# Optimization experiments

Hardware: AMD Instinct MI355X
Metric: run time of the kernel (lower is better)

The kernel has to match this reference:

```python
import jax, jax.numpy as jnp
import numpy as np

S, IN, OUT = 2048, 512, 512
H, KV = 16, 4            # query heads, kv heads (cross-broadcast + averaged)
DQ = DK = DV = 64        # per-head embedding dims


def setup_inputs() -> dict:
    key = jax.random.key(0)
    ks = jax.random.split(key, 5)
    lim_in = 1.0 / np.sqrt(IN)
    lim_o = 1.0 / np.sqrt(H * DV)
    x = jax.random.normal(ks[0], (S, IN), dtype=jnp.float32)
    Wq = jax.random.uniform(ks[1], (H * DQ, IN), jnp.float32, -lim_in, lim_in)
    Wk = jax.random.uniform(ks[2], (KV * DK, IN), jnp.float32, -lim_in, lim_in)
    Wv = jax.random.uniform(ks[3], (KV * DV, IN), jnp.float32, -lim_in, lim_in)
    Wo = jax.random.uniform(ks[4], (OUT, H * DV), jnp.float32, -lim_o, lim_o)
    return {"x": x, "Wq": Wq, "Wk": Wk, "Wv": Wv, "Wo": Wo}


def reference(x, Wq, Wk, Wv, Wo):
    seq = x.shape[0]
    # projections (eqx.nn.Linear: y = W @ x, no bias)
    q = (x @ Wq.T).reshape(seq, H, DQ)    # [S, H, DQ]
    k = (x @ Wk.T).reshape(seq, KV, DK)   # [S, KV, DK]
    v = (x @ Wv.T).reshape(seq, KV, DV)   # [S, KV, DV]
    # cross-broadcast every kv head against every query head -> [KV, H, S, S]
    scores = jnp.einsum('shd,tkd->khst', q, k) / jnp.sqrt(jnp.asarray(DK, x.dtype))
    # NOTE: original applies causal mask whenever `mask is not None`; the
    # boolean flag is always passed, so masking is effectively always on.
    causal = jnp.tril(jnp.ones((seq, seq), dtype=bool))
    scores = jnp.where(causal, scores, -jnp.inf)
    w = jax.nn.softmax(scores, axis=-1)   # [KV, H, S, S]
    # attn @ V, then sum over kv heads and average by KV
    o = jnp.einsum('khst,tkd->shd', w, v) / KV  # [S, H, DV]
    return o.reshape(seq, H * DV) @ Wo.T        # [S, OUT]
```

## Files before the change

kernel.cpp:

```cpp
#include <hip/hip_runtime.h>
#include <hip/hip_bf16.h>

#define SEQ   2048
#define INF_  512
#define HQ    16
#define KVH   4
#define DH    64
#define NQ    (HQ*DH)
#define NKV   (KVH*DH)
#define OUTD  512

typedef short v8s __attribute__((ext_vector_type(8)));
typedef float v4f __attribute__((ext_vector_type(4)));

static __device__ __forceinline__ float bf2f(unsigned short u) {
    union { unsigned int i; float f; } c;
    c.i = ((unsigned int)u) << 16;
    return c.f;
}
static __device__ __forceinline__ unsigned short f2bf(float f) {
    union { float f; unsigned int i; } c; c.f = f;
    unsigned int lsb = (c.i >> 16) & 1u;
    c.i += 0x7fffu + lsb;
    return (unsigned short)(c.i >> 16);
}
static __device__ __forceinline__ unsigned int f2bf2(float lo, float hi) {
    union { __hip_bfloat162 h; unsigned int u; } c;
    c.h = __float22bfloat162_rn(make_float2(lo, hi));
    return c.u;
}
static __device__ __forceinline__ v8s pack8(v4f a, v4f b) {
    union { v8s s; uint4 u; } c;
    c.u = make_uint4(f2bf2(a[0], a[1]), f2bf2(a[2], a[3]),
                     f2bf2(b[0], b[1]), f2bf2(b[2], b[3]));
    return c.s;
}

static __device__ __forceinline__ void gll16(const void* g, void* l) {
    __builtin_amdgcn_global_load_lds(
        (const __attribute__((address_space(1))) void*)g,
        (__attribute__((address_space(3))) void*)l, 16, 0, 0);
}

#define QSCALE 0.180336880f

__global__ __launch_bounds__(256) void cast_all(
    const float* __restrict__ x,  const float* __restrict__ Wq,
    const float* __restrict__ Wk, const float* __restrict__ Wv,
    const float* __restrict__ Wo,
    unsigned short* __restrict__ xb,  unsigned short* __restrict__ Wqb,
    unsigned short* __restrict__ Wkb, unsigned short* __restrict__ Wvb,
    unsigned short* __restrict__ Wob)
{
    size_t i = ((size_t)blockIdx.x * 256 + threadIdx.x) * 8;
    const float* s; unsigned short* d; size_t off;
    if (i < 1048576)      { s = x;  d = xb;  off = i; }
    else if (i < 1572864) { s = Wq; d = Wqb; off = i - 1048576; }
    else if (i < 1703936) { s = Wk; d = Wkb; off = i - 1572864; }
    else if (i < 1835008) { s = Wv; d = Wvb; off = i - 1703936; }
    else                  { s = Wo; d = Wob; off = i - 1835008; }
    float4 a = *(const float4*)(s + off);
    float4 b = *(const float4*)(s + off + 4);
    *(uint4*)(d + off) = make_uint4(f2bf2(a.x, a.y), f2bf2(a.z, a.w),
                                    f2bf2(b.x, b.y), f2bf2(b.z, b.w));
}

__global__ __launch_bounds__(256, 4) void gemm_qkv(
    const unsigned short* __restrict__ xb,
    const unsigned short* __restrict__ Wqb,
    const unsigned short* __restrict__ Wkb,
    const unsigned short* __restrict__ Wvb,
    unsigned short* __restrict__ Qg,
    unsigned short* __restrict__ Kg,
    unsigned short* __restrict__ Vg)
{
    __shared__ unsigned short Asb[64][72];
    __shared__ unsigned short Bsb[64][72];

    const int m0 = blockIdx.x * 64;
    const int n0 = blockIdx.y * 64;

    const unsigned short* Bp; int role;
    if (n0 < NQ)            { Bp = Wqb + (size_t)n0 * INF_;              role = 0; }
    else if (n0 < NQ + NKV) { Bp = Wkb + (size_t)(n0 - NQ) * INF_;       role = 1; }
    else                    { Bp = Wvb + (size_t)(n0 - NQ - NKV) * INF_; role = 2; }

    const int tid = threadIdx.x;
    const int w = tid >> 6, lane = tid & 63;
    const int n = lane & 15, quad = lane >> 4;
    const int r0w = (w & 1) * 32, c0w = (w >> 1) * 32;
    const int sr = tid >> 2, skc = (tid & 3) * 16;

    v4f acc[2][2];
#pragma unroll
    for (int rt = 0; rt < 2; rt++)
#pragma unroll
        for (int ct = 0; ct < 2; ct++) acc[rt][ct] = (v4f){0.f,0.f,0.f,0.f};

    const unsigned short* ap = xb + (size_t)(m0 + sr) * INF_ + skc;
    const unsigned short* bp = Bp + (size_t)sr * INF_ + skc;

    uint4 pa0 = *(const uint4*)(ap),     pa1 = *(const uint4*)(ap + 8);
    uint4 pb0 = *(const uint4*)(bp),     pb1 = *(const uint4*)(bp + 8);

    for (int kb = 0; kb < INF_; kb += 64) {
        __syncthreads();
        *(uint4*)&Asb[sr][skc]     = pa0;
        *(uint4*)&Asb[sr][skc + 8] = pa1;
        *(uint4*)&Bsb[sr][skc]     = pb0;
        *(uint4*)&Bsb[sr][skc + 8] = pb1;
        __syncthreads();
        if (kb + 64 < INF_) {
            pa0 = *(const uint4*)(ap + kb + 64);
            pa1 = *(const uint4*)(ap + kb + 64 + 8);
            pb0 = *(const uint4*)(bp + kb + 64);
            pb1 = *(const uint4*)(bp + kb + 64 + 8);
        }
#pragma unroll
        for (int kk = 0; kk < 2; kk++) {
            v8s a0 = *(const v8s*)&Asb[r0w + n][kk * 32 + quad * 8];
            v8s a1 = *(const v8s*)&Asb[r0w + 16 + n][kk * 32 + quad * 8];
            v8s b0 = *(const v8s*)&Bsb[c0w + n][kk * 32 + quad * 8];
            v8s b1 = *(const v8s*)&Bsb[c0w + 16 + n][kk * 32 + quad * 8];
            acc[0][0] = __builtin_amdgcn_mfma_f32_16x16x32_bf16(a0, b0, acc[0][0], 0, 0, 0);
            acc[0][1] = __builtin_amdgcn_mfma_f32_16x16x32_bf16(a0, b1, acc[0][1], 0, 0, 0);
            acc[1][0] = __builtin_amdgcn_mfma_f32_16x16x32_bf16(a1, b0, acc[1][0], 0, 0, 0);
            acc[1][1] = __builtin_amdgcn_mfma_f32_16x16x32_bf16(a1, b1, acc[1][1], 0, 0, 0);
        }
    }

    const int t = m0 >> 6;
    if (role == 0) {
        unsigned short* base = Qg + ((size_t)(t * 16 + (n0 >> 6))) * 4096;
#pragma unroll
        for (int rt = 0; rt < 2; rt++)
#pragma unroll
            for (int ct = 0; ct < 2; ct++)
#pragma unroll
                for (int reg = 0; reg < 4; reg++) {
                    const int r = r0w + rt * 16 + quad * 4 + reg;
                    const int d = c0w + ct * 16 + n;
                    base[r * 64 + (((d >> 3) ^ (r & 7)) * 8) + (d & 7)] =
                        f2bf(acc[rt][ct][reg] * QSCALE);
                }
    } else if (role == 1) {
        const int g = (n0 - NQ) >> 6;
        unsigned short* base = Kg + ((size_t)(g * 32 + t)) * 4096;
#pragma unroll
        for (int rt = 0; rt < 2; rt++)
#pragma unroll
            for (int ct = 0; ct < 2; ct++)
#pragma unroll
                for (int reg = 0; reg < 4; reg++) {
                    const int r = r0w + rt * 16 + quad * 4 + reg;
                    const int d = c0w + ct * 16 + n;
                    base[r * 64 + (((d >> 3) ^ (r & 7)) * 8) + (d & 7)] =
                        f2bf(acc[rt][ct][reg]);
                }
    } else {
        const int g = (n0 - NQ - NKV) >> 6;
        unsigned short* base = Vg + ((size_t)(g * 32 + t)) * 4096;
#pragma unroll
        for (int rt = 0; rt < 2; rt++)
#pragma unroll
            for (int ct = 0; ct < 2; ct++) {
                const int jb_ = r0w + rt * 16 + quad * 4;
                const int d = c0w + ct * 16 + n;
                const int p = (jb_ & 32) + (((jb_ >> 2) & 3) * 8) + (((jb_ >> 4) & 1) * 4);
                *(uint2*)&base[d * 64 + (((p >> 3) ^ (d & 7)) * 8) + (p & 7)] =
                    make_uint2(f2bf2(acc[rt][ct][0], acc[rt][ct][1]),
                               f2bf2(acc[rt][ct][2], acc[rt][ct][3]));
            }
    }
}

__global__ __launch_bounds__(256, 4) void attn_mfma(
    const unsigned short* __restrict__ Qg,
    const unsigned short* __restrict__ Kg,
    const unsigned short* __restrict__ Vg,
    unsigned short* __restrict__ Oh)
{
    __shared__ unsigned short Ksb[2][4096];
    __shared__ unsigned short Vsb[2][4096];

    const int bx = blockIdx.x;
    const int h  = bx & 15;
    const int jj = (bx >> 4) & 15;
    const int g  = bx >> 8;
    const int jj2 = (jj + 8 * (g >> 1)) & 15;
    const int qi2 = (g & 1) ? (15 - jj2) : jj2;
    const int q0 = qi2 * 128;
    const int tid = threadIdx.x;
    const int w = tid >> 6, lane = tid & 63;
    const int n = lane & 15, quad = lane >> 4;
    const int r0 = w * 32;
    const int m7 = n & 7;
    const int ntile = 2 * qi2 + 2;

    {
        const size_t off = ((size_t)(g * 32)) * 4096 + w * 1024 + lane * 8;
        gll16(Kg + off,       &Ksb[0][w * 1024]);
        gll16(Kg + off + 512, &Ksb[0][w * 1024 + 512]);
        gll16(Vg + off,       &Vsb[0][w * 1024]);
        gll16(Vg + off + 512, &Vsb[0][w * 1024 + 512]);
    }

    v8s qf[2][2];
    {
        const unsigned short* tb =
            Qg + ((size_t)((2 * qi2 + (r0 >> 6)) * 16 + h)) * 4096 + (r0 & 63) * 64;
#pragma unroll
        for (int qt = 0; qt < 2; qt++) {
            const unsigned short* rp = tb + (qt * 16 + n) * 64;
            qf[qt][0] = *(const v8s*)(rp + (quad ^ m7) * 8);
            qf[qt][1] = *(const v8s*)(rp + ((quad + 4) ^ m7) * 8);
        }
    }

    float lst[2] = {0.f, 0.f};
    v4f Oacc[2][4];
#pragma unroll
    for (int qt = 0; qt < 2; qt++)
#pragma unroll
        for (int dt = 0; dt < 4; dt++) Oacc[qt][dt] = (v4f){0.f,0.f,0.f,0.f};
    const v4f z = (v4f){0.f,0.f,0.f,0.f};

    for (int tt = 0; tt < ntile; tt++) {
        const int buf = tt & 1;
        __syncthreads();
        if (tt + 1 < ntile) {
            const size_t off = ((size_t)(g * 32 + tt + 1)) * 4096 + w * 1024 + lane * 8;
            const int nb = buf ^ 1;
            gll16(Kg + off,       &Ksb[nb][w * 1024]);
            gll16(Kg + off + 512, &Ksb[nb][w * 1024 + 512]);
            gll16(Vg + off,       &Vsb[nb][w * 1024]);
            gll16(Vg + off + 512, &Vsb[nb][w * 1024 + 512]);
        }
        const int t0 = tt * 64;
        const bool do0 = (t0 <= q0 + r0 + 15);
        const bool do1 = (t0 <= q0 + r0 + 31);
        if (!do1) continue;

        const unsigned short* Kb = Ksb[buf];
        const unsigned short* Vb = Vsb[buf];

        v4f sc[2][4];
#pragma unroll
        for (int jt = 0; jt < 4; jt++) {
            const int kr = (jt * 16 + n) * 64;
            v8s kf0 = *(const v8s*)&Kb[kr + (quad ^ m7) * 8];
            v8s kf1 = *(const v8s*)&Kb[kr + ((quad + 4) ^ m7) * 8];
            if (do0) {
                v4f tq = __builtin_amdgcn_mfma_f32_16x16x32_bf16(kf0, qf[0][0], z, 0, 0, 0);
                sc[0][jt] = __builtin_amdgcn_mfma_f32_16x16x32_bf16(kf1, qf[0][1], tq, 0, 0, 0);
            }
            v4f t1 = __builtin_amdgcn_mfma_f32_16x16x32_bf16(kf0, qf[1][0], z, 0, 0, 0);
            sc[1][jt] = __builtin_amdgcn_mfma_f32_16x16x32_bf16(kf1, qf[1][1], t1, 0, 0, 0);
        }

#pragma unroll
        for (int qt = 0; qt < 2; qt++) {
            if (qt == 0 && !do0) continue;
            const int qg = q0 + r0 + qt * 16 + n;
            if (t0 + 63 > q0 + r0 + qt * 16) {
#pragma unroll
                for (int jt = 0; jt < 4; jt++) {
                    const int jg = t0 + jt * 16 + quad * 4;
#pragma unroll
                    for (int reg = 0; reg < 4; reg++)
                        sc[qt][jt][reg] = (jg + reg <= qg) ? sc[qt][jt][reg] : -INFINITY;
                }
            }
#pragma unroll
            for (int jt = 0; jt < 4; jt++) {
#pragma unroll
                for (int reg = 0; reg < 4; reg++) {
                    float p = __builtin_amdgcn_exp2f(sc[qt][jt][reg]);
                    sc[qt][jt][reg] = p;
                    lst[qt] += p;
                }
            }
        }

        v8s pf[2][2];
        if (do0) {
            pf[0][0] = pack8(sc[0][0], sc[0][1]);
            pf[0][1] = pack8(sc[0][2], sc[0][3]);
        }
        pf[1][0] = pack8(sc[1][0], sc[1][1]);
        pf[1][1] = pack8(sc[1][2], sc[1][3]);

#pragma unroll
        for (int dt = 0; dt < 4; dt++) {
            const int vr = (dt * 16 + n) * 64;
            v8s vf0 = *(const v8s*)&Vb[vr + (quad ^ m7) * 8];
            v8s vf1 = *(const v8s*)&Vb[vr + ((quad + 4) ^ m7) * 8];
            if (do0) {
                Oacc[0][dt] = __builtin_amdgcn_mfma_f32_16x16x32_bf16(vf0, pf[0][0], Oacc[0][dt], 0, 0, 0);
                Oacc[0][dt] = __builtin_amdgcn_mfma_f32_16x16x32_bf16(vf1, pf[0][1], Oacc[0][dt], 0, 0, 0);
            }
            Oacc[1][dt] = __builtin_amdgcn_mfma_f32_16x16x32_bf16(vf0, pf[1][0], Oacc[1][dt], 0, 0, 0);
            Oacc[1][dt] = __builtin_amdgcn_mfma_f32_16x16x32_bf16(vf1, pf[1][1], Oacc[1][dt], 0, 0, 0);
        }
    }

    unsigned short* Ohp = Oh + (size_t)g * ((size_t)SEQ * NQ);
#pragma unroll
    for (int qt = 0; qt < 2; qt++) {
        float L = lst[qt];
        L += __shfl_xor(L, 16);
        L += __shfl_xor(L, 32);
        const float inv = 0.25f / L;
        const int row = q0 + r0 + qt * 16 + n;
        unsigned short* dst = Ohp + (size_t)row * NQ + h * DH + quad * 4;
#pragma unroll
        for (int dt = 0; dt < 4; dt++) {
            uint2 pk = make_uint2(f2bf2(Oacc[qt][dt][0] * inv, Oacc[qt][dt][1] * inv),
                                  f2bf2(Oacc[qt][dt][2] * inv, Oacc[qt][dt][3] * inv));
            *(uint2*)(dst + dt * 16) = pk;
        }
    }
}

__global__ __launch_bounds__(256, 4) void gemm_out(
    const unsigned short* __restrict__ Oh,
    const unsigned short* __restrict__ Wob,
    float* __restrict__ C)
{
    __shared__ unsigned short Asb[32][72];
    __shared__ unsigned short Bsb[64][72];

    const int m0 = blockIdx.x * 32;
    const int n0 = blockIdx.y * 64;
    const int tid = threadIdx.x;
    const int w = tid >> 6, lane = tid & 63;
    const int n = lane & 15, quad = lane >> 4;
    const int rw = (w & 1) * 16, cw = (w >> 1) * 32;
    const int ar = tid >> 3, akc = (tid & 7) * 8;
    const int br = tid >> 2, bkc = (tid & 3) * 16;

    v4f acc[2];
    acc[0] = (v4f){0.f,0.f,0.f,0.f};
    acc[1] = (v4f){0.f,0.f,0.f,0.f};

    const size_t plane = (size_t)SEQ * NQ;
    const size_t abase = (size_t)(m0 + ar) * NQ + akc;
    const unsigned short* bp = Wob + (size_t)(n0 + br) * NQ + bkc;

    uint4 ua[4];
#pragma unroll
    for (int g = 0; g < 4; g++) ua[g] = *(const uint4*)(Oh + g * plane + abase);
    uint4 ub0 = *(const uint4*)(bp), ub1 = *(const uint4*)(bp + 8);

    for (int kb = 0; kb < NQ; kb += 64) {
        __syncthreads();
        {
            unsigned int ow[4];
#pragma unroll
            for (int q = 0; q < 4; q++) {
                const unsigned int u0 = ((const unsigned int*)&ua[0])[q];
                const unsigned int u1 = ((const unsigned int*)&ua[1])[q];
                const unsigned int u2 = ((const unsigned int*)&ua[2])[q];
                const unsigned int u3 = ((const unsigned int*)&ua[3])[q];
                float lo = bf2f((unsigned short)(u0 & 0xffffu)) + bf2f((unsigned short)(u1 & 0xffffu))
                         + bf2f((unsigned short)(u2 & 0xffffu)) + bf2f((unsigned short)(u3 & 0xffffu));
                float hi = bf2f((unsigned short)(u0 >> 16)) + bf2f((unsigned short)(u1 >> 16))
                         + bf2f((unsigned short)(u2 >> 16)) + bf2f((unsigned short)(u3 >> 16));
                ow[q] = f2bf2(lo, hi);
            }
            *(uint4*)&Asb[ar][akc] = make_uint4(ow[0], ow[1], ow[2], ow[3]);
        }
        *(uint4*)&Bsb[br][bkc]     = ub0;
        *(uint4*)&Bsb[br][bkc + 8] = ub1;
        __syncthreads();
        if (kb + 64 < NQ) {
#pragma unroll
            for (int g = 0; g < 4; g++)
                ua[g] = *(const uint4*)(Oh + g * plane + abase + kb + 64);
            ub0 = *(const uint4*)(bp + kb + 64);
            ub1 = *(const uint4*)(bp + kb + 64 + 8);
        }
#pragma unroll
        for (int kk = 0; kk < 2; kk++) {
            v8s a  = *(const v8s*)&Asb[rw + n][kk * 32 + quad * 8];
            v8s b0 = *(const v8s*)&Bsb[cw + n][kk * 32 + quad * 8];
            v8s b1 = *(const v8s*)&Bsb[cw + 16 + n][kk * 32 + quad * 8];
            acc[0] = __builtin_amdgcn_mfma_f32_16x16x32_bf16(a, b0, acc[0], 0, 0, 0);
            acc[1] = __builtin_amdgcn_mfma_f32_16x16x32_bf16(a, b1, acc[1], 0, 0, 0);
        }
    }

#pragma unroll
    for (int ct = 0; ct < 2; ct++)
#pragma unroll
        for (int reg = 0; reg < 4; reg++) {
            const int row = m0 + rw + quad * 4 + reg;
            const int col = n0 + cw + ct * 16 + n;
            C[(size_t)row * OUTD + col] = acc[ct][reg];
        }
}

extern "C" void kernel_launch(void* const* d_in, const int* in_sizes, int n_in,
                              void* d_out, int out_size, void* d_ws, size_t ws_size,
                              hipStream_t stream) {
    const float* x  = (const float*)d_in[0];
    const float* Wq = (const float*)d_in[1];
    const float* Wk = (const float*)d_in[2];
    const float* Wv = (const float*)d_in[3];
    const float* Wo = (const float*)d_in[4];
    float* out = (float*)d_out;

    char* base = (char*)d_ws;
    unsigned short* Oh  = (unsigned short*)(base);
    unsigned short* xb  = (unsigned short*)(base);
    unsigned short* Wqb = (unsigned short*)(base + 2097152);
    unsigned short* Wkb = (unsigned short*)(base + 3145728);
    unsigned short* Wvb = (unsigned short*)(base + 3407872);
    unsigned short* Qg  = (unsigned short*)(base + 16777216);
    unsigned short* Kg  = (unsigned short*)(base + 20971520);
    unsigned short* Vg  = (unsigned short*)(base + 22020096);
    unsigned short* Wob = (unsigned short*)(base + 23068672);

    dim3 blk(256);
    cast_all<<<dim3(1152), blk, 0, stream>>>(x, Wq, Wk, Wv, Wo,
                                             xb, Wqb, Wkb, Wvb, Wob);
    gemm_qkv<<<dim3(SEQ / 64, (NQ + 2 * NKV) / 64), blk, 0, stream>>>(
        xb, Wqb, Wkb, Wvb, Qg, Kg, Vg);
    attn_mfma<<<dim3(1024), blk, 0, stream>>>(Qg, Kg, Vg, Oh);
    gemm_out<<<dim3(SEQ / 32, OUTD / 64), blk, 0, stream>>>(Oh, Wob, out);
}
```

Baseline: 155.6 us.

## Use async global-to-LDS double buffering in QKV GEMM and MFMA row sums in attention

```diff
diff --git a/kernel.cpp b/kernel.cpp
--- a/kernel.cpp
+++ b/kernel.cpp
@@ -40,6 +40,19 @@
     __builtin_amdgcn_global_load_lds(
         (const __attribute__((address_space(1))) void*)g,
         (__attribute__((address_space(3))) void*)l, 16, 0, 0);
+}
+
+static __device__ __forceinline__ void stage_tile(
+    const unsigned short* __restrict__ src, int stride, int kb,
+    unsigned short* ldsbase, int w, int lane)
+{
+#pragma unroll
+    for (int i = 0; i < 2; i++) {
+        const int rl = w * 16 + i * 8 + (lane >> 3);
+        const int kc = ((lane & 7) ^ (rl & 7)) * 8;
+        gll16(src + (size_t)rl * stride + kb + kc,
+              ldsbase + (w * 16 + i * 8) * 64);
+    }
 }
 
 #define QSCALE 0.180336880f
@@ -74,8 +87,8 @@
     unsigned short* __restrict__ Kg,
     unsigned short* __restrict__ Vg)
 {
-    __shared__ unsigned short Asb[64][72];
-    __shared__ unsigned short Bsb[64][72];
+    __shared__ unsigned short Asb[2][4096];
+    __shared__ unsigned short Bsb[2][4096];
 
     const int m0 = blockIdx.x * 64;
     const int n0 = blockIdx.y * 64;
@@ -88,8 +101,9 @@
     const int tid = threadIdx.x;
     const int w = tid >> 6, lane = tid & 63;
     const int n = lane & 15, quad = lane >> 4;
+    const int m7 = n & 7;
     const int r0w = (w & 1) * 32, c0w = (w >> 1) * 32;
-    const int sr = tid >> 2, skc = (tid & 3) * 16;
+    const unsigned short* Ap = xb + (size_t)m0 * INF_;
 
     v4f acc[2][2];
 #pragma unroll
@@ -97,31 +111,23 @@
 #pragma unroll
         for (int ct = 0; ct < 2; ct++) acc[rt][ct] = (v4f){0.f,0.f,0.f,0.f};
 
-    const unsigned short* ap = xb + (size_t)(m0 + sr) * INF_ + skc;
-    const unsigned short* bp = Bp + (size_t)sr * INF_ + skc;
-
-    uint4 pa0 = *(const uint4*)(ap),     pa1 = *(const uint4*)(ap + 8);
-    uint4 pb0 = *(const uint4*)(bp),     pb1 = *(const uint4*)(bp + 8);
+    stage_tile(Ap, INF_, 0, &Asb[0][0], w, lane);
+    stage_tile(Bp, INF_, 0, &Bsb[0][0], w, lane);
 
     for (int kb = 0; kb < INF_; kb += 64) {
-        __syncthreads();
-        *(uint4*)&Asb[sr][skc]     = pa0;
-        *(uint4*)&Asb[sr][skc + 8] = pa1;
-        *(uint4*)&Bsb[sr][skc]     = pb0;
-        *(uint4*)&Bsb[sr][skc + 8] = pb1;
+        const int buf = (kb >> 6) & 1;
         __syncthreads();
         if (kb + 64 < INF_) {
-            pa0 = *(const uint4*)(ap + kb + 64);
-            pa1 = *(const uint4*)(ap + kb + 64 + 8);
-            pb0 = *(const uint4*)(bp + kb + 64);
-            pb1 = *(const uint4*)(bp + kb + 64 + 8);
+            stage_tile(Ap, INF_, kb + 64, &Asb[buf ^ 1][0], w, lane);
+            stage_tile(Bp, INF_, kb + 64, &Bsb[buf ^ 1][0], w, lane);
         }
 #pragma unroll
         for (int kk = 0; kk < 2; kk++) {
-            v8s a0 = *(const v8s*)&Asb[r0w + n][kk * 32 + quad * 8];
-            v8s a1 = *(const v8s*)&Asb[r0w + 16 + n][kk * 32 + quad * 8];
-            v8s b0 = *(const v8s*)&Bsb[c0w + n][kk * 32 + quad * 8];
-            v8s b1 = *(const v8s*)&Bsb[c0w + 16 + n][kk * 32 + quad * 8];
+            const int gs = ((kk * 4 + quad) ^ m7) * 8;
+            v8s a0 = *(const v8s*)&Asb[buf][(r0w + n) * 64 + gs];
+            v8s a1 = *(const v8s*)&Asb[buf][(r0w + 16 + n) * 64 + gs];
+            v8s b0 = *(const v8s*)&Bsb[buf][(c0w + n) * 64 + gs];
+            v8s b1 = *(const v8s*)&Bsb[buf][(c0w + 16 + n) * 64 + gs];
             acc[0][0] = __builtin_amdgcn_mfma_f32_16x16x32_bf16(a0, b0, acc[0][0], 0, 0, 0);
             acc[0][1] = __builtin_amdgcn_mfma_f32_16x16x32_bf16(a0, b1, acc[0][1], 0, 0, 0);
             acc[1][0] = __builtin_amdgcn_mfma_f32_16x16x32_bf16(a1, b0, acc[1][0], 0, 0, 0);
@@ -217,7 +223,13 @@
         }
     }
 
-    float lst[2] = {0.f, 0.f};
+    v8s ones;
+#pragma unroll
+    for (int i = 0; i < 8; i++) ones[i] = (short)0x3F80;
+
+    v4f Lacc[2];
+    Lacc[0] = (v4f){0.f,0.f,0.f,0.f};
+    Lacc[1] = (v4f){0.f,0.f,0.f,0.f};
     v4f Oacc[2][4];
 #pragma unroll
     for (int qt = 0; qt < 2; qt++)
@@ -272,14 +284,10 @@
                 }
             }
 #pragma unroll
-            for (int jt = 0; jt < 4; jt++) {
-#pragma unroll
-                for (int reg = 0; reg < 4; reg++) {
-                    float p = __builtin_amdgcn_exp2f(sc[qt][jt][reg]);
-                    sc[qt][jt][reg] = p;
-                    lst[qt] += p;
-                }
-            }
+            for (int jt = 0; jt < 4; jt++)
+#pragma unroll
+                for (int reg = 0; reg < 4; reg++)
+                    sc[qt][jt][reg] = __builtin_amdgcn_exp2f(sc[qt][jt][reg]);
         }
 
         v8s pf[2][2];
@@ -289,6 +297,13 @@
         }
         pf[1][0] = pack8(sc[1][0], sc[1][1]);
         pf[1][1] = pack8(sc[1][2], sc[1][3]);
+
+        if (do0) {
+            Lacc[0] = __builtin_amdgcn_mfma_f32_16x16x32_bf16(ones, pf[0][0], Lacc[0], 0, 0, 0);
+            Lacc[0] = __builtin_amdgcn_mfma_f32_16x16x32_bf16(ones, pf[0][1], Lacc[0], 0, 0, 0);
+        }
+        Lacc[1] = __builtin_amdgcn_mfma_f32_16x16x32_bf16(ones, pf[1][0], Lacc[1], 0, 0, 0);
+        Lacc[1] = __builtin_amdgcn_mfma_f32_16x16x32_bf16(ones, pf[1][1], Lacc[1], 0, 0, 0);
 
 #pragma unroll
         for (int dt = 0; dt < 4; dt++) {
@@ -307,10 +322,7 @@
     unsigned short* Ohp = Oh + (size_t)g * ((size_t)SEQ * NQ);
 #pragma unroll
     for (int qt = 0; qt < 2; qt++) {
-        float L = lst[qt];
-        L += __shfl_xor(L, 16);
-        L += __shfl_xor(L, 32);
-        const float inv = 0.25f / L;
+        const float inv = 0.25f / Lacc[qt][0];
         const int row = q0 + r0 + qt * 16 + n;
         unsigned short* dst = Ohp + (size_t)row * NQ + h * DH + quad * 4;
 #pragma unroll
```

New measurement: 142.0 us. 8.7% less time.
